# Kernel tuning notes

Measured on AMD Instinct MI355X. Metric: run time of the kernel, lower is better.

Reference implementation:

```python
import jax, jax.numpy as jnp
import numpy as np

MARGIN = 0.3
HARD_FACTOR = 0.0
EPS = 1e-6


def setup_inputs() -> dict:
    key = jax.random.key(0)
    k1, k2 = jax.random.split(key)
    inputs = jax.random.normal(k1, (4096, 256), dtype=jnp.float32)
    targets = jax.random.randint(k2, (4096,), 0, 512, dtype=jnp.int64)
    return {"inputs": inputs, "targets": targets}


def reference(inputs, targets):
    n = inputs.shape[0]
    half = n // 2
    # L2-normalize features (matches normalize(): x / (||x|| + 1e-6))
    x = inputs / (jnp.linalg.norm(inputs, axis=-1, keepdims=True) + EPS)
    # pairwise euclidean distances, clamped at 1e-6 before sqrt
    sq = jnp.sum(x * x, axis=1)                      # (n,)
    dist = sq[:, None] + sq[None, :] - 2.0 * (x @ x.T)  # (n, n)
    dist = jnp.sqrt(jnp.clip(dist, EPS))
    # same-identity mask
    mask = targets[:, None] == targets[None, :]      # (n, n) bool
    # rows in the first half mine over columns [half:n], rows in the
    # second half mine over columns [0:half] -> gather the opposite half
    first = (jnp.arange(n) < half)[:, None]          # (n, 1)
    d_o = jnp.where(first, dist[:, half:], dist[:, :half])  # (n, half)
    m_o = jnp.where(first, mask[:, half:], mask[:, :half])  # (n, half) bool
    pos_any = jnp.any(m_o, axis=1)
    neg_any = jnp.any(~m_o, axis=1)
    dist_ap = jnp.where(pos_any,
                        jnp.max(jnp.where(m_o, d_o, -jnp.inf), axis=1),
                        0.0)
    dist_an = jnp.where(neg_any,
                        jnp.min(jnp.where(m_o, jnp.inf, d_o), axis=1),
                        1.0)
    dist_ap = dist_ap * (1.0 + HARD_FACTOR)
    dist_an = dist_an * (1.0 - HARD_FACTOR)
    # MarginRankingLoss(margin)(dist_an, dist_ap, y=1) =
    #   mean(relu(-(dist_an - dist_ap) + margin))
    loss = jnp.mean(jax.nn.relu(dist_ap - dist_an + MARGIN))
    return loss
```

## Files before the change

kernel.cpp:

```cpp
#include <hip/hip_runtime.h>
#include <hip/hip_bf16.h>
#include <math.h>

#define N 4096
#define D 256
#define HALF 2048
#define MARGIN 0.3f

#define BM 64
#define BK 32
#define LDB 40

typedef __attribute__((ext_vector_type(8))) short bf16x8;
typedef __attribute__((ext_vector_type(4))) float f32x4;

__global__ __launch_bounds__(256) void k_norm(const float* __restrict__ in,
                                              unsigned short* __restrict__ xnb,
                                              float* __restrict__ sq,
                                              int* __restrict__ ap,
                                              int* __restrict__ an) {
    const int row = blockIdx.x;
    const int t = threadIdx.x;
    float v = in[(size_t)row * D + t];
    float s = v * v;
#pragma unroll
    for (int o = 32; o > 0; o >>= 1) s += __shfl_down(s, o, 64);
    __shared__ float wsum[4];
    __shared__ float inv_s, sq_s;
    if ((t & 63) == 0) wsum[t >> 6] = s;
    __syncthreads();
    if (t == 0) {
        float tot = wsum[0] + wsum[1] + wsum[2] + wsum[3];
        float nrm = sqrtf(tot);
        float inv = 1.0f / (nrm + 1e-6f);
        inv_s = inv;
        float q = nrm * inv;
        sq_s = q * q;
    }
    __syncthreads();
    float x = v * inv_s;
    unsigned int u = __float_as_uint(x);
    xnb[(size_t)row * D + t] =
        (unsigned short)((u + 0x7fffu + ((u >> 16) & 1u)) >> 16);
    if (t == 0) {
        sq[row] = sq_s;
        ap[row] = 0;
        an[row] = 0x7f800000;
    }
}

__global__ __launch_bounds__(256) void k_tile(const unsigned short* __restrict__ xnb,
                                              const float* __restrict__ sq,
                                              const int* __restrict__ tg,
                                              int* __restrict__ ap,
                                              int* __restrict__ an) {
    __shared__ unsigned short As[BM * LDB];
    __shared__ unsigned short Bs[BM * LDB];
    __shared__ int sra[BM], srn[BM], sca[BM], scn[BM];

    const int bi = blockIdx.y, bj = blockIdx.x;
    const int I0 = bi * BM;
    const int J0 = bj * BM;
    const int tid = threadIdx.x;
    const int wave = tid >> 6, lane = tid & 63;
    const int wm = wave >> 1, wn = wave & 1;
    const int lrow = lane & 15, lquad = lane >> 4;

    f32x4 acc[2][2];
#pragma unroll
    for (int a = 0; a < 2; ++a)
#pragma unroll
        for (int b = 0; b < 2; ++b) acc[a][b] = (f32x4){0.f, 0.f, 0.f, 0.f};

    const unsigned short* Ag = xnb + (size_t)I0 * D;
    const unsigned short* Bg = xnb + (size_t)(HALF + J0) * D;
    const int srow = tid >> 2, sseg = tid & 3;

    for (int k0 = 0; k0 < D; k0 += BK) {
        __syncthreads();
        *(uint4*)&As[srow * LDB + sseg * 8] =
            *(const uint4*)&Ag[(size_t)srow * D + k0 + sseg * 8];
        *(uint4*)&Bs[srow * LDB + sseg * 8] =
            *(const uint4*)&Bg[(size_t)srow * D + k0 + sseg * 8];
        __syncthreads();
        bf16x8 af[2], bfr[2];
#pragma unroll
        for (int mi = 0; mi < 2; ++mi)
            af[mi] = *(const bf16x8*)&As[(wm * 32 + mi * 16 + lrow) * LDB + lquad * 8];
#pragma unroll
        for (int nj = 0; nj < 2; ++nj)
            bfr[nj] = *(const bf16x8*)&Bs[(wn * 32 + nj * 16 + lrow) * LDB + lquad * 8];
#pragma unroll
        for (int mi = 0; mi < 2; ++mi)
#pragma unroll
            for (int nj = 0; nj < 2; ++nj)
                acc[mi][nj] = __builtin_amdgcn_mfma_f32_16x16x32_bf16(
                    af[mi], bfr[nj], acc[mi][nj], 0, 0, 0);
    }

    float sqi[2][4], sqj[2];
    int tgi[2][4], tgj[2];
#pragma unroll
    for (int mi = 0; mi < 2; ++mi)
#pragma unroll
        for (int r = 0; r < 4; ++r) {
            int gi = I0 + wm * 32 + mi * 16 + lquad * 4 + r;
            sqi[mi][r] = sq[gi];
            tgi[mi][r] = tg[gi];
        }
#pragma unroll
    for (int nj = 0; nj < 2; ++nj) {
        int gj = HALF + J0 + wn * 32 + nj * 16 + lrow;
        sqj[nj] = sq[gj];
        tgj[nj] = tg[gj];
    }

    const float INF = __int_as_float(0x7f800000);
    float rap[2][4], ran[2][4], capv[2], canv[2];
#pragma unroll
    for (int mi = 0; mi < 2; ++mi)
#pragma unroll
        for (int r = 0; r < 4; ++r) { rap[mi][r] = 0.f; ran[mi][r] = INF; }
#pragma unroll
    for (int nj = 0; nj < 2; ++nj) { capv[nj] = 0.f; canv[nj] = INF; }

#pragma unroll
    for (int mi = 0; mi < 2; ++mi)
#pragma unroll
        for (int nj = 0; nj < 2; ++nj)
#pragma unroll
            for (int r = 0; r < 4; ++r) {
                float d2 = sqi[mi][r] + sqj[nj] - 2.0f * acc[mi][nj][r];
                float d = sqrtf(fmaxf(d2, 1e-6f));
                if (tgi[mi][r] == tgj[nj]) {
                    rap[mi][r] = fmaxf(rap[mi][r], d);
                    capv[nj] = fmaxf(capv[nj], d);
                } else {
                    ran[mi][r] = fminf(ran[mi][r], d);
                    canv[nj] = fminf(canv[nj], d);
                }
            }

#pragma unroll
    for (int mi = 0; mi < 2; ++mi)
#pragma unroll
        for (int r = 0; r < 4; ++r) {
#pragma unroll
            for (int o = 1; o < 16; o <<= 1) {
                rap[mi][r] = fmaxf(rap[mi][r], __shfl_xor(rap[mi][r], o, 64));
                ran[mi][r] = fminf(ran[mi][r], __shfl_xor(ran[mi][r], o, 64));
            }
        }
#pragma unroll
    for (int nj = 0; nj < 2; ++nj) {
#pragma unroll
        for (int o = 16; o < 64; o <<= 1) {
            capv[nj] = fmaxf(capv[nj], __shfl_xor(capv[nj], o, 64));
            canv[nj] = fminf(canv[nj], __shfl_xor(canv[nj], o, 64));
        }
    }

    if (tid < BM) { sra[tid] = 0; srn[tid] = 0x7f800000;
                    sca[tid] = 0; scn[tid] = 0x7f800000; }
    __syncthreads();
    if (lrow == 0) {
#pragma unroll
        for (int mi = 0; mi < 2; ++mi)
#pragma unroll
            for (int r = 0; r < 4; ++r) {
                int lr = wm * 32 + mi * 16 + lquad * 4 + r;
                atomicMax(&sra[lr], __float_as_int(rap[mi][r]));
                atomicMin(&srn[lr], __float_as_int(ran[mi][r]));
            }
    }
    if (lquad == 0) {
#pragma unroll
        for (int nj = 0; nj < 2; ++nj) {
            int lc = wn * 32 + nj * 16 + lrow;
            atomicMax(&sca[lc], __float_as_int(capv[nj]));
            atomicMin(&scn[lc], __float_as_int(canv[nj]));
        }
    }
    __syncthreads();
    if (tid < BM) {
        atomicMax(&ap[I0 + tid], sra[tid]);
        atomicMin(&an[I0 + tid], srn[tid]);
        atomicMax(&ap[HALF + J0 + tid], sca[tid]);
        atomicMin(&an[HALF + J0 + tid], scn[tid]);
    }
}

__global__ __launch_bounds__(1024) void k_loss(const int* __restrict__ ap,
                                               const int* __restrict__ an,
                                               float* __restrict__ out) {
    const int t = threadIdx.x;
    float s = 0.f;
#pragma unroll
    for (int i = t; i < N; i += 1024) {
        float dap = __int_as_float(ap[i]);
        int anb = an[i];
        float dan = (anb == 0x7f800000) ? 1.0f : __int_as_float(anb);
        float v = dap - dan + MARGIN;
        s += (v > 0.f) ? v : 0.f;
    }
#pragma unroll
    for (int o = 32; o > 0; o >>= 1) s += __shfl_down(s, o, 64);
    __shared__ float wsum[16];
    if ((t & 63) == 0) wsum[t >> 6] = s;
    __syncthreads();
    if (t == 0) {
        float tot = 0.f;
#pragma unroll
        for (int w = 0; w < 16; ++w) tot += wsum[w];
        out[0] = tot / (float)N;
    }
}

extern "C" void kernel_launch(void* const* d_in, const int* in_sizes, int n_in,
                              void* d_out, int out_size, void* d_ws, size_t ws_size,
                              hipStream_t stream) {
    const float* in = (const float*)d_in[0];
    const int* tg = (const int*)d_in[1];
    float* out = (float*)d_out;

    unsigned short* xnb = (unsigned short*)d_ws;
    float* sq = (float*)(xnb + (size_t)N * D);
    int* ap = (int*)(sq + N);
    int* an = ap + N;

    k_norm<<<N, 256, 0, stream>>>(in, xnb, sq, ap, an);
    k_tile<<<dim3(HALF / BM, HALF / BM), 256, 0, stream>>>(xnb, sq, tg, ap, an);
    k_loss<<<1, 1024, 0, stream>>>(ap, an, out);
}
```

Measured before the change: 73.18 us.

## Load full K tiles via direct global-to-LDS with XOR swizzle; one row per wave in norm

The tile kernel now copies the whole 64x256 A and B panels into LDS up front with global_load_lds 16-byte transfers, using an XOR swizzle to avoid bank conflicts. This removes the eight sync-separated K iterations and the register staging. The norm kernel processes one row per wave with float4 loads and no block-level syncs. The trade is 64KB of LDS per block, which caps occupancy at about two blocks per CU, and the per-row reduction scratch now reuses the A panel.

```diff
diff --git a/kernel.cpp b/kernel.cpp
--- a/kernel.cpp
+++ b/kernel.cpp
@@ -1,5 +1,4 @@
 #include <hip/hip_runtime.h>
-#include <hip/hip_bf16.h>
 #include <math.h>
 
 #define N 4096
@@ -8,55 +7,56 @@
 #define MARGIN 0.3f
 
 #define BM 64
-#define BK 32
-#define LDB 40
 
 typedef __attribute__((ext_vector_type(8))) short bf16x8;
 typedef __attribute__((ext_vector_type(4))) float f32x4;
+
+typedef __attribute__((address_space(1))) const unsigned int gas_uint;
+typedef __attribute__((address_space(3))) unsigned int las_uint;
+
+__device__ __forceinline__ void gld16(const unsigned short* g, unsigned short* l) {
+    __builtin_amdgcn_global_load_lds((gas_uint*)g, (las_uint*)l, 16, 0, 0);
+}
+
+__device__ __forceinline__ unsigned short f2bf(float x) {
+    unsigned int u = __float_as_uint(x);
+    return (unsigned short)((u + 0x7fffu + ((u >> 16) & 1u)) >> 16);
+}
 
 __global__ __launch_bounds__(256) void k_norm(const float* __restrict__ in,
                                               unsigned short* __restrict__ xnb,
                                               float* __restrict__ sq,
                                               int* __restrict__ ap,
                                               int* __restrict__ an) {
-    const int row = blockIdx.x;
-    const int t = threadIdx.x;
-    float v = in[(size_t)row * D + t];
-    float s = v * v;
-#pragma unroll
-    for (int o = 32; o > 0; o >>= 1) s += __shfl_down(s, o, 64);
-    __shared__ float wsum[4];
-    __shared__ float inv_s, sq_s;
-    if ((t & 63) == 0) wsum[t >> 6] = s;
-    __syncthreads();
-    if (t == 0) {
-        float tot = wsum[0] + wsum[1] + wsum[2] + wsum[3];
-        float nrm = sqrtf(tot);
-        float inv = 1.0f / (nrm + 1e-6f);
-        inv_s = inv;
+    const int row = blockIdx.x * 4 + (threadIdx.x >> 6);
+    const int lane = threadIdx.x & 63;
+    const float4 v = *(const float4*)&in[(size_t)row * D + lane * 4];
+    float s = v.x * v.x + v.y * v.y + v.z * v.z + v.w * v.w;
+#pragma unroll
+    for (int o = 1; o < 64; o <<= 1) s += __shfl_xor(s, o, 64);
+    float nrm = sqrtf(s);
+    float inv = 1.0f / (nrm + 1e-6f);
+    ushort4 o4;
+    o4.x = f2bf(v.x * inv);
+    o4.y = f2bf(v.y * inv);
+    o4.z = f2bf(v.z * inv);
+    o4.w = f2bf(v.w * inv);
+    *(ushort4*)&xnb[(size_t)row * D + lane * 4] = o4;
+    if (lane == 0) {
         float q = nrm * inv;
-        sq_s = q * q;
-    }
-    __syncthreads();
-    float x = v * inv_s;
-    unsigned int u = __float_as_uint(x);
-    xnb[(size_t)row * D + t] =
-        (unsigned short)((u + 0x7fffu + ((u >> 16) & 1u)) >> 16);
-    if (t == 0) {
-        sq[row] = sq_s;
+        sq[row] = q * q;
         ap[row] = 0;
         an[row] = 0x7f800000;
     }
 }
 
-__global__ __launch_bounds__(256) void k_tile(const unsigned short* __restrict__ xnb,
-                                              const float* __restrict__ sq,
-                                              const int* __restrict__ tg,
-                                              int* __restrict__ ap,
-                                              int* __restrict__ an) {
-    __shared__ unsigned short As[BM * LDB];
-    __shared__ unsigned short Bs[BM * LDB];
-    __shared__ int sra[BM], srn[BM], sca[BM], scn[BM];
+__global__ __launch_bounds__(256, 2) void k_tile(const unsigned short* __restrict__ xnb,
+                                                 const float* __restrict__ sq,
+                                                 const int* __restrict__ tg,
+                                                 int* __restrict__ ap,
+                                                 int* __restrict__ an) {
+    __shared__ unsigned short As[BM * D];
+    __shared__ unsigned short Bs[BM * D];
 
     const int bi = blockIdx.y, bj = blockIdx.x;
     const int I0 = bi * BM;
@@ -66,30 +66,42 @@
     const int wm = wave >> 1, wn = wave & 1;
     const int lrow = lane & 15, lquad = lane >> 4;
 
-    f32x4 acc[2][2];
-#pragma unroll
-    for (int a = 0; a < 2; ++a)
-#pragma unroll
-        for (int b = 0; b < 2; ++b) acc[a][b] = (f32x4){0.f, 0.f, 0.f, 0.f};
-
     const unsigned short* Ag = xnb + (size_t)I0 * D;
     const unsigned short* Bg = xnb + (size_t)(HALF + J0) * D;
-    const int srow = tid >> 2, sseg = tid & 3;
-
-    for (int k0 = 0; k0 < D; k0 += BK) {
-        __syncthreads();
-        *(uint4*)&As[srow * LDB + sseg * 8] =
-            *(const uint4*)&Ag[(size_t)srow * D + k0 + sseg * 8];
-        *(uint4*)&Bs[srow * LDB + sseg * 8] =
-            *(const uint4*)&Bg[(size_t)srow * D + k0 + sseg * 8];
-        __syncthreads();
+
+#pragma unroll
+    for (int i = 0; i < 8; ++i) {
+        const int ch = i * 4 + wave;
+        const int e = ch * 64 + lane;
+        const int row = e >> 5;
+        const int sc = (e & 31) ^ (row & 7);
+        gld16(Ag + row * D + sc * 8, &As[ch * 512]);
+        gld16(Bg + row * D + sc * 8, &Bs[ch * 512]);
+    }
+    asm volatile("s_waitcnt vmcnt(0)" ::: "memory");
+    __syncthreads();
+
+    f32x4 acc[2][2];
+#pragma unroll
+    for (int a = 0; a < 2; ++a)
+#pragma unroll
+        for (int b = 0; b < 2; ++b) acc[a][b] = (f32x4){0.f, 0.f, 0.f, 0.f};
+
+#pragma unroll
+    for (int kk = 0; kk < 8; ++kk) {
         bf16x8 af[2], bfr[2];
 #pragma unroll
-        for (int mi = 0; mi < 2; ++mi)
-            af[mi] = *(const bf16x8*)&As[(wm * 32 + mi * 16 + lrow) * LDB + lquad * 8];
-#pragma unroll
-        for (int nj = 0; nj < 2; ++nj)
-            bfr[nj] = *(const bf16x8*)&Bs[(wn * 32 + nj * 16 + lrow) * LDB + lquad * 8];
+        for (int mi = 0; mi < 2; ++mi) {
+            const int r = wm * 32 + mi * 16 + lrow;
+            const int s = r * 32 + ((kk * 4 + lquad) ^ (r & 7));
+            af[mi] = *(const bf16x8*)&As[s * 8];
+        }
+#pragma unroll
+        for (int nj = 0; nj < 2; ++nj) {
+            const int r = wn * 32 + nj * 16 + lrow;
+            const int s = r * 32 + ((kk * 4 + lquad) ^ (r & 7));
+            bfr[nj] = *(const bf16x8*)&Bs[s * 8];
+        }
 #pragma unroll
         for (int mi = 0; mi < 2; ++mi)
 #pragma unroll
@@ -160,6 +172,12 @@
         }
     }
 
+    int* sra = (int*)As;
+    int* srn = sra + BM;
+    int* sca = srn + BM;
+    int* scn = sca + BM;
+
+    __syncthreads();
     if (tid < BM) { sra[tid] = 0; srn[tid] = 0x7f800000;
                     sca[tid] = 0; scn[tid] = 0x7f800000; }
     __syncthreads();
@@ -228,7 +246,7 @@
     int* ap = (int*)(sq + N);
     int* an = ap + N;
 
-    k_norm<<<N, 256, 0, stream>>>(in, xnb, sq, ap, an);
+    k_norm<<<N / 4, 256, 0, stream>>>(in, xnb, sq, ap, an);
     k_tile<<<dim3(HALF / BM, HALF / BM), 256, 0, stream>>>(xnb, sq, tg, ap, an);
     k_loss<<<1, 1024, 0, stream>>>(ap, an, out);
 }
```

After: 73.47 us. Within noise of the previous version (+0.4%).
